# Kernel optimization log

Measured on AMD Instinct MI355X. Metric: run time of the kernel, lower is better.

## Reference

```python
import jax, jax.numpy as jnp
import numpy as np

N = 100000   # nodes
E = 1000000  # edges
DS = 16      # stage start/end scale-out vec dim
DC = 224     # raw context dim
CC = DS + DC + DS  # context_channels = 256
DM = 128     # stage_metrics_channels
H = (CC + DM) // 2  # 192 hidden of final_transform
OUT = 128    # out_channels (== DM, required by overwrite path)


def setup_inputs() -> dict:
    key = jax.random.key(0)
    ks = jax.random.split(key, 16)
    n = lambda k, shape, s=0.05: jax.random.normal(k, shape, jnp.float32) * s
    return {
        "edge_index": jax.random.randint(ks[0], (2, E), 0, N, dtype=jnp.int64),
        "stage_start": jax.random.normal(ks[1], (N, DS), jnp.float32),
        "stage_end": jax.random.normal(ks[2], (N, DS), jnp.float32),
        "context": jax.random.normal(ks[3], (N, DC), jnp.float32),
        "stage_metrics": jax.random.normal(ks[4], (N, DM), jnp.float32),
        "W_l": n(ks[5], (CC, CC)), "b_l": jnp.zeros((CC,), jnp.float32),
        "W_r": n(ks[6], (CC, CC)), "b_r": jnp.zeros((CC,), jnp.float32),
        "att": n(ks[7], (CC,)),
        "W1": n(ks[8], (CC + DM, H)), "b1": jnp.zeros((H,), jnp.float32),
        "W2": n(ks[9], (H, OUT)), "b2": jnp.zeros((OUT,), jnp.float32),
        "bias": jnp.zeros((OUT,), jnp.float32),
    }


def reference(edge_index, stage_start, stage_end, context, stage_metrics,
              W_l, b_l, W_r, b_r, att, W1, b1, W2, b2, bias):
    # node transform: [N, CC]
    nc = jnp.concatenate([stage_start, context, stage_end], axis=-1)
    cl = nc @ W_l + b_l  # source-side (j)
    cr = nc @ W_r + b_r  # target-side (i)

    src, dst = edge_index[0], edge_index[1]  # flow: source_to_target, aggregate by dst
    ci = cr[dst]                 # [E, CC] context_i
    cj = cl[src]                 # [E, CC] context_j
    mj = stage_metrics[src]      # [E, DM] metrics_j

    ctx = jax.nn.selu(ci + cj)
    ctx = jnp.where(jnp.all(mj == 0, axis=1, keepdims=True), 0.0, ctx)

    alpha = ctx @ att            # [E]
    mask = alpha != 0            # ~zero_indices

    # segment softmax over non-zero alphas, grouped by dst (PyG softmax: sub max, exp, /sum+eps)
    NEG = jnp.float32(-1e30)
    m = jax.ops.segment_max(jnp.where(mask, alpha, NEG), dst, num_segments=N)
    ex = jnp.where(mask, jnp.exp(alpha - m[dst]), 0.0)
    s = jax.ops.segment_sum(ex, dst, num_segments=N)
    a = jnp.where(mask, ex / (s[dst] + 1e-16), 0.0)

    # per-edge 2-layer SELU MLP
    h = jax.nn.selu(jnp.concatenate([ctx, mj], axis=-1) @ W1 + b1)  # [E, H]
    f = jax.nn.selu(h @ W2 + b2)                                    # [E, OUT]
    msg = jnp.where(mask[:, None], f * a[:, None], 0.0)

    # scatter-add aggregation to nodes
    out = jax.ops.segment_sum(msg, dst, num_segments=N)  # [N, OUT]

    # rows with all-zero aggregation are overwritten by stage_metrics; others get bias + sigmoid
    ovr = jnp.all(out == 0, axis=1, keepdims=True)
    return jnp.where(ovr, stage_metrics, jax.nn.sigmoid(out + bias))
```

## Files before the change

kernel.cpp:

```cpp
#include <hip/hip_runtime.h>
#include <hip/hip_bf16.h>
#include <math.h>

#define NN   100000
#define EE   1000000
#define CCH  256
#define DMC  128
#define HDC  192
#define OUTC 128
#define ET   32
#define MS   132
#define GS   391

typedef unsigned short u16;
using bf16x8 = __attribute__((ext_vector_type(8))) short;
using f32x4  = __attribute__((ext_vector_type(4))) float;
using u16x4  = __attribute__((ext_vector_type(4))) unsigned short;
using u16x8  = __attribute__((ext_vector_type(8))) unsigned short;

__device__ __forceinline__ float selu_f(float x) {
    const float sc = 1.0507009873554804934193349852946f;
    const float c1 = 1.7580993408473765792727863477367f;
    const float e = __expf(x);
    return x > 0.0f ? sc * x : __builtin_fmaf(c1, e, -c1);
}
__device__ __forceinline__ u16 f2bf(float f) {
    union { __hip_bfloat16 h; u16 u; } c;
    c.h = __float2bfloat16(f);
    return c.u;
}
__device__ __forceinline__ float bf2f(u16 h) {
    return __uint_as_float(((unsigned int)h) << 16);
}

__global__ __launch_bounds__(256, 2) void k_node_gemm(
    const float* __restrict__ ss, const float* __restrict__ se,
    const float* __restrict__ ctx, const u16* __restrict__ W0p,
    const float* __restrict__ bl, const float* __restrict__ br,
    u16* __restrict__ clb, u16* __restrict__ crb)
{
    __shared__ __align__(16) char Xs[64 * 512];
    const int tid = threadIdx.x;
    const int wave = tid >> 6, lane = tid & 63;
    const int node0 = blockIdx.x * 64;

    {
        const int r = lane;
        const int nd = min(node0 + r, NN - 1);
#pragma unroll
        for (int i = 0; i < 8; ++i) {
            const int c0 = wave * 64 + i * 8;
            float4 va, vb;
            {
                const int c = c0;
                if (c < 16)       va = *reinterpret_cast<const float4*>(ss + nd * 16 + c);
                else if (c < 240) va = *reinterpret_cast<const float4*>(ctx + (size_t)nd * 224 + (c - 16));
                else              va = *reinterpret_cast<const float4*>(se + nd * 16 + (c - 240));
            }
            {
                const int c = c0 + 4;
                if (c < 16)       vb = *reinterpret_cast<const float4*>(ss + nd * 16 + c);
                else if (c < 240) vb = *reinterpret_cast<const float4*>(ctx + (size_t)nd * 224 + (c - 16));
                else              vb = *reinterpret_cast<const float4*>(se + nd * 16 + (c - 240));
            }
            u16x8 v;
            v[0] = f2bf(va.x); v[1] = f2bf(va.y); v[2] = f2bf(va.z); v[3] = f2bf(va.w);
            v[4] = f2bf(vb.x); v[5] = f2bf(vb.y); v[6] = f2bf(vb.z); v[7] = f2bf(vb.w);
            *reinterpret_cast<u16x8*>(Xs + r * 512 + ((c0 * 2) ^ ((r & 7) << 4))) = v;
        }
    }
    __syncthreads();

    const int r16   = lane & 15;
    const int khalf = (lane >> 4) << 4;
    const int rbase = (lane >> 4) * 4;

    f32x4 acc[4][8];
#pragma unroll
    for (int m = 0; m < 4; ++m)
#pragma unroll
        for (int jj = 0; jj < 8; ++jj) acc[m][jj] = (f32x4){0.f, 0.f, 0.f, 0.f};

    for (int ks = 0; ks < 8; ++ks) {
        bf16x8 b[8];
#pragma unroll
        for (int jj = 0; jj < 8; ++jj)
            b[jj] = *reinterpret_cast<const bf16x8*>(
                W0p + (((size_t)(wave + 4 * jj) * 8 + ks) * 64 + lane) * 8);
        const int kb = ks * 64 + khalf;
#pragma unroll
        for (int m = 0; m < 4; ++m) {
            const int row = m * 16 + r16;
            const bf16x8 a = *reinterpret_cast<const bf16x8*>(
                Xs + row * 512 + (kb ^ ((row & 7) << 4)));
#pragma unroll
            for (int jj = 0; jj < 8; ++jj)
                acc[m][jj] = __builtin_amdgcn_mfma_f32_16x16x32_bf16(a, b[jj], acc[m][jj], 0, 0, 0);
        }
    }

#pragma unroll
    for (int jj = 0; jj < 8; ++jj) {
        const int nt = wave + 4 * jj;
        const bool isL = nt < 16;
        const int ncl = (isL ? nt * 16 : (nt - 16) * 16) + r16;
        const float bias = isL ? bl[ncl] : br[ncl];
        u16* base = (isL ? clb : crb) + ncl;
#pragma unroll
        for (int m = 0; m < 4; ++m)
#pragma unroll
            for (int rr = 0; rr < 4; ++rr) {
                const int node = node0 + m * 16 + rbase + rr;
                if (node < NN)
                    base[(size_t)node * CCH] = f2bf(acc[m][jj][rr] + bias);
            }
    }
}

__global__ __launch_bounds__(256) void k_convert(
    const float* __restrict__ in, u16* __restrict__ out, int n)
{
    const int i = (blockIdx.x * 256 + threadIdx.x) * 4;
    if (i < n) {
        const float4 v = *reinterpret_cast<const float4*>(in + i);
        u16x4 o; o[0] = f2bf(v.x); o[1] = f2bf(v.y); o[2] = f2bf(v.z); o[3] = f2bf(v.w);
        *reinterpret_cast<u16x4*>(out + i) = o;
    }
}

__global__ __launch_bounds__(64) void k_pack_w(
    const float* __restrict__ W, u16* __restrict__ out, int K, int N)
{
    const int f = blockIdx.x, lane = threadIdx.x;
    const int KS = K >> 5;
    const int nt = f / KS, ks = f - nt * KS;
    const int n = nt * 16 + (lane & 15);
    const int k0 = ks * 32 + (lane >> 4) * 8;
    u16x8 v;
#pragma unroll
    for (int j = 0; j < 8; ++j) v[j] = f2bf(W[(size_t)(k0 + j) * N + n]);
    *reinterpret_cast<u16x8*>(out + ((size_t)f * 64 + lane) * 8) = v;
}

__global__ __launch_bounds__(64) void k_pack_att(
    const float* __restrict__ att, u16* __restrict__ attp)
{
    const int ks = blockIdx.x;
    const int lane = threadIdx.x;
    const int nloc = lane & 15;
    const int k0 = ks * 32 + (lane >> 4) * 8;
    u16x8 v;
#pragma unroll
    for (int j = 0; j < 8; ++j) v[j] = f2bf((nloc == 0) ? att[k0 + j] : 0.f);
    *reinterpret_cast<u16x8*>(attp + ((size_t)ks * 64 + lane) * 8) = v;
}

__global__ __launch_bounds__(256) void k_hist(
    const int* __restrict__ ei, int* __restrict__ cnt)
{
    const int i = blockIdx.x * 256 + threadIdx.x;
    if (i < EE / 4) {
        const int4 d = *reinterpret_cast<const int4*>(ei + EE + i * 4);
        atomicAdd(&cnt[d.x], 1); atomicAdd(&cnt[d.y], 1);
        atomicAdd(&cnt[d.z], 1); atomicAdd(&cnt[d.w], 1);
    }
}

__global__ __launch_bounds__(256) void k_scan1(
    const int* __restrict__ cnt, int* __restrict__ bsum)
{
    const int i = blockIdx.x * 256 + threadIdx.x;
    int v = (i < NN) ? cnt[i] : 0;
#pragma unroll
    for (int o = 1; o < 64; o <<= 1) v += __shfl_xor(v, o);
    __shared__ int ws[4];
    if ((threadIdx.x & 63) == 0) ws[threadIdx.x >> 6] = v;
    __syncthreads();
    if (threadIdx.x == 0) bsum[blockIdx.x] = ws[0] + ws[1] + ws[2] + ws[3];
}

__global__ __launch_bounds__(512) void k_scan2(int* __restrict__ bsum)
{
    __shared__ int s[512];
    const int t = threadIdx.x;
    const int v = (t < GS) ? bsum[t] : 0;
    s[t] = v;
    __syncthreads();
    for (int o = 1; o < 512; o <<= 1) {
        const int u = (t >= o) ? s[t - o] : 0;
        __syncthreads();
        s[t] += u;
        __syncthreads();
    }
    if (t < GS) bsum[t] = s[t] - v;
}

__global__ __launch_bounds__(256) void k_scan3(
    const int* __restrict__ cnt, const int* __restrict__ bsum,
    int* __restrict__ cur)
{
    const int t = threadIdx.x;
    const int i = blockIdx.x * 256 + t;
    const int lane = t & 63, w = t >> 6;
    const int v = (i < NN) ? cnt[i] : 0;
    int x = v;
#pragma unroll
    for (int o = 1; o < 64; o <<= 1) {
        const int u = __shfl_up(x, o);
        if (lane >= o) x += u;
    }
    __shared__ int wsum[4];
    if (lane == 63) wsum[w] = x;
    __syncthreads();
    int off = bsum[blockIdx.x];
    for (int k2 = 0; k2 < w; ++k2) off += wsum[k2];
    if (i < NN) cur[i] = off + x - v;
}

__global__ __launch_bounds__(256) void k_scatter(
    const int* __restrict__ ei, int* __restrict__ cur,
    int* __restrict__ srcs, int* __restrict__ dsts)
{
    const int i = blockIdx.x * 256 + threadIdx.x;
    if (i < EE) {
        const int d = ei[EE + i];
        const int pos = atomicAdd(&cur[d], 1);
        srcs[pos] = ei[i];
        dsts[pos] = d;
    }
}

__global__ __launch_bounds__(256, 6) void k_edge_mlp(
    const int* __restrict__ srcs, const int* __restrict__ dsts,
    const u16* __restrict__ clb, const u16* __restrict__ crb,
    const u16* __restrict__ metb, const u16* __restrict__ attp,
    float* __restrict__ sb,
    const u16* __restrict__ W1p, const float* __restrict__ b1,
    const u16* __restrict__ W2p, const float* __restrict__ b2,
    float* __restrict__ dout)
{
    __shared__ __align__(16) char Xs[ET * 768];
    __shared__ int esrc[ET], edst[ET], flg[ET];
    __shared__ float exs[ET];

    const int tid  = threadIdx.x;
    const int wave = tid >> 6;
    const int lane = tid & 63;
    const int ebase = blockIdx.x * ET;

    if (tid < ET) {
        esrc[tid] = srcs[ebase + tid];
        edst[tid] = dsts[ebase + tid];
    }
    __syncthreads();

    u16x8 rv[4], lv[4], mv[2];
#pragma unroll
    for (int i = 0; i < 4; ++i) {
        const int k = tid + i * 256;
        const int t = k >> 5, c = k & 31;
        rv[i] = *reinterpret_cast<const u16x8*>(crb + (size_t)edst[t] * CCH + c * 8);
        lv[i] = *reinterpret_cast<const u16x8*>(clb + (size_t)esrc[t] * CCH + c * 8);
    }
#pragma unroll
    for (int i = 0; i < 2; ++i) {
        const int k = tid + i * 256;
        mv[i] = *reinterpret_cast<const u16x8*>(metb + (size_t)esrc[k >> 4] * DMC + (k & 15) * 8);
    }
#pragma unroll
    for (int i = 0; i < 4; ++i) {
        const int k = tid + i * 256;
        const int t = k >> 5, c = k & 31;
        u16x8 v;
#pragma unroll
        for (int j = 0; j < 8; ++j) v[j] = f2bf(selu_f(bf2f(rv[i][j]) + bf2f(lv[i][j])));
        *reinterpret_cast<u16x8*>(Xs + t * 768 + ((c * 16) ^ ((t & 7) << 4))) = v;
    }
#pragma unroll
    for (int i = 0; i < 2; ++i) {
        const int k = tid + i * 256;
        const int t = k >> 4, g = k & 15;
        unsigned ob = 0;
#pragma unroll
        for (int j = 0; j < 8; ++j) ob |= (unsigned)mv[i][j];
        const bool nz = (ob & 0x7fffu) != 0u;
        const unsigned long long bal = __ballot(nz);
        if ((lane & 15) == 0)
            flg[t] = (int)((bal >> ((lane >> 4) * 16)) & 0xFFFFull) != 0;
        *reinterpret_cast<u16x8*>(Xs + t * 768 + (((32 + g) * 16) ^ ((t & 7) << 4))) = mv[i];
    }
    __syncthreads();

    const int r16   = lane & 15;
    const int khalf = (lane >> 4) << 4;
    const int rbase = (lane >> 4) * 4;

    f32x4 acc[2][3];
    f32x4 acc3[2];
#pragma unroll
    for (int m = 0; m < 2; ++m) {
#pragma unroll
        for (int j = 0; j < 3; ++j) acc[m][j] = (f32x4){0.f, 0.f, 0.f, 0.f};
        acc3[m] = (f32x4){0.f, 0.f, 0.f, 0.f};
    }

    for (int ks = 0; ks < 12; ++ks) {
        bf16x8 b[3];
#pragma unroll
        for (int j = 0; j < 3; ++j)
            b[j] = *reinterpret_cast<const bf16x8*>(
                W1p + (((size_t)(wave + 4 * j) * 12 + ks) * 64 + lane) * 8);
        bf16x8 b3 = {};
        const bool doA = (wave == 0) && (ks < 8);
        if (doA)
            b3 = *reinterpret_cast<const bf16x8*>(attp + ((size_t)ks * 64 + lane) * 8);
        const int kb = ks * 64 + khalf;
#pragma unroll
        for (int m = 0; m < 2; ++m) {
            const int row = m * 16 + r16;
            const bf16x8 a = *reinterpret_cast<const bf16x8*>(
                Xs + row * 768 + (kb ^ ((row & 7) << 4)));
#pragma unroll
            for (int j = 0; j < 3; ++j)
                acc[m][j] = __builtin_amdgcn_mfma_f32_16x16x32_bf16(a, b[j], acc[m][j], 0, 0, 0);
            if (doA)
                acc3[m] = __builtin_amdgcn_mfma_f32_16x16x32_bf16(a, b3, acc3[m], 0, 0, 0);
        }
    }

    if (wave == 0 && r16 == 0) {
        const int hi = lane >> 4;
#pragma unroll
        for (int m = 0; m < 2; ++m)
#pragma unroll
            for (int r = 0; r < 4; ++r) {
                const int e = m * 16 + hi * 4 + r;
                const float al = acc3[m][r];
                exs[e] = (flg[e] && al != 0.f) ? __expf(al) : 0.f;
            }
    }
    __syncthreads();

#pragma unroll
    for (int j = 0; j < 3; ++j) {
        const int n = (wave + 4 * j) * 16 + r16;
        const float bb = b1[n];
#pragma unroll
        for (int m = 0; m < 2; ++m)
#pragma unroll
            for (int r = 0; r < 4; ++r) {
                const int row = m * 16 + rbase + r;
                *reinterpret_cast<u16*>(Xs + row * 384 + ((n * 2) ^ ((row & 7) << 4))) =
                    f2bf(selu_f(acc[m][j][r] + bb));
            }
    }
    __syncthreads();

    f32x4 acc2[2][2];
#pragma unroll
    for (int m = 0; m < 2; ++m)
#pragma unroll
        for (int j = 0; j < 2; ++j) acc2[m][j] = (f32x4){0.f, 0.f, 0.f, 0.f};

    for (int ks = 0; ks < 6; ++ks) {
        bf16x8 b[2];
#pragma unroll
        for (int j = 0; j < 2; ++j)
            b[j] = *reinterpret_cast<const bf16x8*>(
                W2p + (((size_t)(wave + 4 * j) * 6 + ks) * 64 + lane) * 8);
        const int kb = ks * 64 + khalf;
#pragma unroll
        for (int m = 0; m < 2; ++m) {
            const int row = m * 16 + r16;
            const bf16x8 a = *reinterpret_cast<const bf16x8*>(
                Xs + row * 384 + (kb ^ ((row & 7) << 4)));
#pragma unroll
            for (int j = 0; j < 2; ++j)
                acc2[m][j] = __builtin_amdgcn_mfma_f32_16x16x32_bf16(a, b[j], acc2[m][j], 0, 0, 0);
        }
    }
    __syncthreads();

    float* Ms = (float*)Xs;
#pragma unroll
    for (int j = 0; j < 2; ++j) {
        const int n = (wave + 4 * j) * 16 + r16;
        const float bb = b2[n];
#pragma unroll
        for (int m = 0; m < 2; ++m)
#pragma unroll
            for (int r = 0; r < 4; ++r) {
                const int e = m * 16 + rbase + r;
                Ms[e * MS + n] = selu_f(acc2[m][j][r] + bb) * exs[e];
            }
    }
    if (tid < ET) Ms[tid * MS + 128] = exs[tid];
    __syncthreads();

    {
        const int col = tid & 127;
        const int h = tid >> 7;
        const int r0 = h * 16;
        int cur_d = edst[r0];
        float s = Ms[r0 * MS + col];
        for (int r = r0 + 1; r < r0 + 16; ++r) {
            const int d = edst[r];
            const float v = Ms[r * MS + col];
            if (d != cur_d) {
                if (s != 0.f) atomicAdd(&dout[(size_t)cur_d * OUTC + col], s);
                cur_d = d; s = v;
            } else {
                s += v;
            }
        }
        if (s != 0.f) atomicAdd(&dout[(size_t)cur_d * OUTC + col], s);
    }
    if (tid < 2) {
        const int r0 = tid * 16;
        int cur_d = edst[r0];
        float s = Ms[r0 * MS + 128];
        for (int r = r0 + 1; r < r0 + 16; ++r) {
            const int d = edst[r];
            const float v = Ms[r * MS + 128];
            if (d != cur_d) {
                if (s != 0.f) atomicAdd(&sb[cur_d], s);
                cur_d = d; s = v;
            } else {
                s += v;
            }
        }
        if (s != 0.f) atomicAdd(&sb[cur_d], s);
    }
}

__global__ __launch_bounds__(256) void k_finalize(
    float* __restrict__ dout, const float* __restrict__ met,
    const float* __restrict__ bias, const float* __restrict__ sb)
{
    const int n = blockIdx.x * 4 + (threadIdx.x >> 6);
    const int lane = threadIdx.x & 63;
    const float a0 = dout[(size_t)n * OUTC + lane];
    const float a1 = dout[(size_t)n * OUTC + 64 + lane];
    const bool ovr = __all((a0 == 0.f) && (a1 == 0.f));
    float r0, r1;
    if (ovr) {
        r0 = met[(size_t)n * DMC + lane];
        r1 = met[(size_t)n * DMC + 64 + lane];
    } else {
        const float inv = 1.0f / (sb[n] + 1e-16f);
        r0 = 1.f / (1.f + __expf(-(a0 * inv + bias[lane])));
        r1 = 1.f / (1.f + __expf(-(a1 * inv + bias[64 + lane])));
    }
    dout[(size_t)n * OUTC + lane] = r0;
    dout[(size_t)n * OUTC + 64 + lane] = r1;
}

extern "C" void kernel_launch(void* const* d_in, const int* in_sizes, int n_in,
                              void* d_out, int out_size, void* d_ws, size_t ws_size,
                              hipStream_t stream)
{
    const int*   ei   = (const int*)d_in[0];
    const float* ss   = (const float*)d_in[1];
    const float* se   = (const float*)d_in[2];
    const float* ctx  = (const float*)d_in[3];
    const float* met  = (const float*)d_in[4];
    const float* Wl   = (const float*)d_in[5];
    const float* bl   = (const float*)d_in[6];
    const float* Wr   = (const float*)d_in[7];
    const float* br   = (const float*)d_in[8];
    const float* att  = (const float*)d_in[9];
    const float* W1   = (const float*)d_in[10];
    const float* b1   = (const float*)d_in[11];
    const float* W2   = (const float*)d_in[12];
    const float* b2   = (const float*)d_in[13];
    const float* bias = (const float*)d_in[14];

    u16* clb  = (u16*)d_ws;
    u16* crb  = clb  + (size_t)NN * CCH;
    u16* metb = crb  + (size_t)NN * CCH;
    u16* W1p  = metb + (size_t)NN * DMC;
    u16* W2p  = W1p  + (size_t)(CCH + DMC) * HDC;
    u16* W0p  = W2p  + (size_t)HDC * OUTC;
    float* sb = (float*)(W0p + (size_t)CCH * 512);
    int* cnt  = (int*)(sb + NN);
    int* cur  = cnt + NN;
    int* srcs = cur + NN;
    int* dsts = srcs + EE;
    int* bsum = dsts + EE;
    u16* attp = (u16*)(bsum + 512);

    float* dout = (float*)d_out;

    hipMemsetAsync(dout, 0, (size_t)NN * OUTC * sizeof(float), stream);
    hipMemsetAsync(sb, 0, (size_t)NN * sizeof(float), stream);
    hipMemsetAsync(cnt, 0, (size_t)NN * sizeof(int), stream);

    k_hist<<<(EE / 4 + 255) / 256, 256, 0, stream>>>(ei, cnt);
    k_scan1<<<GS, 256, 0, stream>>>(cnt, bsum);
    k_scan2<<<1, 512, 0, stream>>>(bsum);
    k_scan3<<<GS, 256, 0, stream>>>(cnt, bsum, cur);
    k_scatter<<<(EE + 255) / 256, 256, 0, stream>>>(ei, cur, srcs, dsts);

    k_pack_w<<<(CCH / 16) * (CCH / 32), 64, 0, stream>>>(Wl, W0p, CCH, CCH);
    k_pack_w<<<(CCH / 16) * (CCH / 32), 64, 0, stream>>>(Wr, W0p + (size_t)128 * 64 * 8, CCH, CCH);
    k_pack_w<<<(HDC / 16) * ((CCH + DMC) / 32), 64, 0, stream>>>(W1, W1p, CCH + DMC, HDC);
    k_pack_w<<<(OUTC / 16) * (HDC / 32), 64, 0, stream>>>(W2, W2p, HDC, OUTC);
    k_pack_att<<<8, 64, 0, stream>>>(att, attp);
    k_convert<<<(NN * DMC / 4 + 255) / 256, 256, 0, stream>>>(met, metb, NN * DMC);

    k_node_gemm<<<(NN + 63) / 64, 256, 0, stream>>>(ss, se, ctx, W0p, bl, br, clb, crb);
    k_edge_mlp<<<EE / ET, 256, 0, stream>>>(srcs, dsts, clb, crb, metb, attp, sb,
                                            W1p, b1, W2p, b2, dout);
    k_finalize<<<NN / 4, 256, 0, stream>>>(dout, met, bias, sb);
}
```

Baseline: 706.0 us.

## Double edge tile to 64 with 8-wave 2x4 layout and merge prep kernels

The edge MLP kernel now processes 64 edges per block with 512 threads arranged as a 2x4 wave grid. Each block's W1, W2 and att fragment loads are therefore shared across twice as many edges, cutting weight traffic per edge. Separately, the src/dst arrays are packed into int2, the four weight-pack launches and the att-pack launch are merged into one kernel, and two adjacent memsets are combined, all to save launches and loads. The larger tile doubles LDS use per block, which can lower how many blocks fit on a CU.

```diff
diff --git a/kernel.cpp b/kernel.cpp
--- a/kernel.cpp
+++ b/kernel.cpp
@@ -8,7 +8,7 @@
 #define DMC  128
 #define HDC  192
 #define OUTC 128
-#define ET   32
+#define ET   64
 #define MS   132
 #define GS   391
 
@@ -128,10 +128,10 @@
     }
 }
 
-__global__ __launch_bounds__(64) void k_pack_w(
-    const float* __restrict__ W, u16* __restrict__ out, int K, int N)
-{
-    const int f = blockIdx.x, lane = threadIdx.x;
+__device__ __forceinline__ void pack_frag(
+    const float* __restrict__ W, u16* __restrict__ out, int K, int N,
+    int f, int lane)
+{
     const int KS = K >> 5;
     const int nt = f / KS, ks = f - nt * KS;
     const int n = nt * 16 + (lane & 15);
@@ -142,17 +142,27 @@
     *reinterpret_cast<u16x8*>(out + ((size_t)f * 64 + lane) * 8) = v;
 }
 
-__global__ __launch_bounds__(64) void k_pack_att(
-    const float* __restrict__ att, u16* __restrict__ attp)
-{
-    const int ks = blockIdx.x;
-    const int lane = threadIdx.x;
-    const int nloc = lane & 15;
-    const int k0 = ks * 32 + (lane >> 4) * 8;
-    u16x8 v;
-#pragma unroll
-    for (int j = 0; j < 8; ++j) v[j] = f2bf((nloc == 0) ? att[k0 + j] : 0.f);
-    *reinterpret_cast<u16x8*>(attp + ((size_t)ks * 64 + lane) * 8) = v;
+__global__ __launch_bounds__(64) void k_pack_all(
+    const float* __restrict__ Wl, const float* __restrict__ Wr,
+    const float* __restrict__ W1, const float* __restrict__ W2,
+    const float* __restrict__ att,
+    u16* __restrict__ W0p, u16* __restrict__ W1p, u16* __restrict__ W2p,
+    u16* __restrict__ attp)
+{
+    const int b = blockIdx.x, lane = threadIdx.x;
+    if (b < 128)       pack_frag(Wl, W0p, CCH, CCH, b, lane);
+    else if (b < 256)  pack_frag(Wr, W0p + (size_t)128 * 64 * 8, CCH, CCH, b - 128, lane);
+    else if (b < 400)  pack_frag(W1, W1p, CCH + DMC, HDC, b - 256, lane);
+    else if (b < 448)  pack_frag(W2, W2p, HDC, OUTC, b - 400, lane);
+    else {
+        const int ks = b - 448;
+        const int nloc = lane & 15;
+        const int k0 = ks * 32 + (lane >> 4) * 8;
+        u16x8 v;
+#pragma unroll
+        for (int j = 0; j < 8; ++j) v[j] = f2bf((nloc == 0) ? att[k0 + j] : 0.f);
+        *reinterpret_cast<u16x8*>(attp + ((size_t)ks * 64 + lane) * 8) = v;
+    }
 }
 
 __global__ __launch_bounds__(256) void k_hist(
@@ -218,20 +228,18 @@
 }
 
 __global__ __launch_bounds__(256) void k_scatter(
-    const int* __restrict__ ei, int* __restrict__ cur,
-    int* __restrict__ srcs, int* __restrict__ dsts)
+    const int* __restrict__ ei, int* __restrict__ cur, int2* __restrict__ sd)
 {
     const int i = blockIdx.x * 256 + threadIdx.x;
     if (i < EE) {
         const int d = ei[EE + i];
         const int pos = atomicAdd(&cur[d], 1);
-        srcs[pos] = ei[i];
-        dsts[pos] = d;
-    }
-}
-
-__global__ __launch_bounds__(256, 6) void k_edge_mlp(
-    const int* __restrict__ srcs, const int* __restrict__ dsts,
+        sd[pos] = make_int2(ei[i], d);
+    }
+}
+
+__global__ __launch_bounds__(512, 6) void k_edge_mlp(
+    const int2* __restrict__ sd,
     const u16* __restrict__ clb, const u16* __restrict__ crb,
     const u16* __restrict__ metb, const u16* __restrict__ attp,
     float* __restrict__ sb,
@@ -246,30 +254,32 @@
     const int tid  = threadIdx.x;
     const int wave = tid >> 6;
     const int lane = tid & 63;
+    const int wm = wave >> 2, wn = wave & 3;
     const int ebase = blockIdx.x * ET;
 
     if (tid < ET) {
-        esrc[tid] = srcs[ebase + tid];
-        edst[tid] = dsts[ebase + tid];
+        const int2 p = sd[ebase + tid];
+        esrc[tid] = p.x;
+        edst[tid] = p.y;
     }
     __syncthreads();
 
     u16x8 rv[4], lv[4], mv[2];
 #pragma unroll
     for (int i = 0; i < 4; ++i) {
-        const int k = tid + i * 256;
+        const int k = tid + i * 512;
         const int t = k >> 5, c = k & 31;
         rv[i] = *reinterpret_cast<const u16x8*>(crb + (size_t)edst[t] * CCH + c * 8);
         lv[i] = *reinterpret_cast<const u16x8*>(clb + (size_t)esrc[t] * CCH + c * 8);
     }
 #pragma unroll
     for (int i = 0; i < 2; ++i) {
-        const int k = tid + i * 256;
+        const int k = tid + i * 512;
         mv[i] = *reinterpret_cast<const u16x8*>(metb + (size_t)esrc[k >> 4] * DMC + (k & 15) * 8);
     }
 #pragma unroll
     for (int i = 0; i < 4; ++i) {
-        const int k = tid + i * 256;
+        const int k = tid + i * 512;
         const int t = k >> 5, c = k & 31;
         u16x8 v;
 #pragma unroll
@@ -278,7 +288,7 @@
     }
 #pragma unroll
     for (int i = 0; i < 2; ++i) {
-        const int k = tid + i * 256;
+        const int k = tid + i * 512;
         const int t = k >> 4, g = k & 15;
         unsigned ob = 0;
 #pragma unroll
@@ -309,15 +319,15 @@
 #pragma unroll
         for (int j = 0; j < 3; ++j)
             b[j] = *reinterpret_cast<const bf16x8*>(
-                W1p + (((size_t)(wave + 4 * j) * 12 + ks) * 64 + lane) * 8);
+                W1p + (((size_t)(wn + 4 * j) * 12 + ks) * 64 + lane) * 8);
         bf16x8 b3 = {};
-        const bool doA = (wave == 0) && (ks < 8);
+        const bool doA = (wn == 0) && (ks < 8);
         if (doA)
             b3 = *reinterpret_cast<const bf16x8*>(attp + ((size_t)ks * 64 + lane) * 8);
         const int kb = ks * 64 + khalf;
 #pragma unroll
         for (int m = 0; m < 2; ++m) {
-            const int row = m * 16 + r16;
+            const int row = (wm * 2 + m) * 16 + r16;
             const bf16x8 a = *reinterpret_cast<const bf16x8*>(
                 Xs + row * 768 + (kb ^ ((row & 7) << 4)));
 #pragma unroll
@@ -328,13 +338,13 @@
         }
     }
 
-    if (wave == 0 && r16 == 0) {
+    if (wn == 0 && r16 == 0) {
         const int hi = lane >> 4;
 #pragma unroll
         for (int m = 0; m < 2; ++m)
 #pragma unroll
             for (int r = 0; r < 4; ++r) {
-                const int e = m * 16 + hi * 4 + r;
+                const int e = (wm * 2 + m) * 16 + hi * 4 + r;
                 const float al = acc3[m][r];
                 exs[e] = (flg[e] && al != 0.f) ? __expf(al) : 0.f;
             }
@@ -343,13 +353,13 @@
 
 #pragma unroll
     for (int j = 0; j < 3; ++j) {
-        const int n = (wave + 4 * j) * 16 + r16;
+        const int n = (wn + 4 * j) * 16 + r16;
         const float bb = b1[n];
 #pragma unroll
         for (int m = 0; m < 2; ++m)
 #pragma unroll
             for (int r = 0; r < 4; ++r) {
-                const int row = m * 16 + rbase + r;
+                const int row = (wm * 2 + m) * 16 + rbase + r;
                 *reinterpret_cast<u16*>(Xs + row * 384 + ((n * 2) ^ ((row & 7) << 4))) =
                     f2bf(selu_f(acc[m][j][r] + bb));
             }
@@ -367,11 +377,11 @@
 #pragma unroll
         for (int j = 0; j < 2; ++j)
             b[j] = *reinterpret_cast<const bf16x8*>(
-                W2p + (((size_t)(wave + 4 * j) * 6 + ks) * 64 + lane) * 8);
+                W2p + (((size_t)(wn + 4 * j) * 6 + ks) * 64 + lane) * 8);
         const int kb = ks * 64 + khalf;
 #pragma unroll
         for (int m = 0; m < 2; ++m) {
-            const int row = m * 16 + r16;
+            const int row = (wm * 2 + m) * 16 + r16;
             const bf16x8 a = *reinterpret_cast<const bf16x8*>(
                 Xs + row * 384 + (kb ^ ((row & 7) << 4)));
 #pragma unroll
@@ -384,13 +394,13 @@
     float* Ms = (float*)Xs;
 #pragma unroll
     for (int j = 0; j < 2; ++j) {
-        const int n = (wave + 4 * j) * 16 + r16;
+        const int n = (wn + 4 * j) * 16 + r16;
         const float bb = b2[n];
 #pragma unroll
         for (int m = 0; m < 2; ++m)
 #pragma unroll
             for (int r = 0; r < 4; ++r) {
-                const int e = m * 16 + rbase + r;
+                const int e = (wm * 2 + m) * 16 + rbase + r;
                 Ms[e * MS + n] = selu_f(acc2[m][j][r] + bb) * exs[e];
             }
     }
@@ -415,7 +425,7 @@
         }
         if (s != 0.f) atomicAdd(&dout[(size_t)cur_d * OUTC + col], s);
     }
-    if (tid < 2) {
+    if (tid < 4) {
         const int r0 = tid * 16;
         int cur_d = edst[r0];
         float s = Ms[r0 * MS + 128];
@@ -484,32 +494,26 @@
     float* sb = (float*)(W0p + (size_t)CCH * 512);
     int* cnt  = (int*)(sb + NN);
     int* cur  = cnt + NN;
-    int* srcs = cur + NN;
-    int* dsts = srcs + EE;
-    int* bsum = dsts + EE;
+    int2* sd  = (int2*)(cur + NN);
+    int* bsum = (int*)(sd + EE);
     u16* attp = (u16*)(bsum + 512);
 
     float* dout = (float*)d_out;
 
     hipMemsetAsync(dout, 0, (size_t)NN * OUTC * sizeof(float), stream);
-    hipMemsetAsync(sb, 0, (size_t)NN * sizeof(float), stream);
-    hipMemsetAsync(cnt, 0, (size_t)NN * sizeof(int), stream);
+    hipMemsetAsync(sb, 0, (size_t)NN * 2 * sizeof(float), stream);
 
     k_hist<<<(EE / 4 + 255) / 256, 256, 0, stream>>>(ei, cnt);
     k_scan1<<<GS, 256, 0, stream>>>(cnt, bsum);
     k_scan2<<<1, 512, 0, stream>>>(bsum);
     k_scan3<<<GS, 256, 0, stream>>>(cnt, bsum, cur);
-    k_scatter<<<(EE + 255) / 256, 256, 0, stream>>>(ei, cur, srcs, dsts);
-
-    k_pack_w<<<(CCH / 16) * (CCH / 32), 64, 0, stream>>>(Wl, W0p, CCH, CCH);
-    k_pack_w<<<(CCH / 16) * (CCH / 32), 64, 0, stream>>>(Wr, W0p + (size_t)128 * 64 * 8, CCH, CCH);
-    k_pack_w<<<(HDC / 16) * ((CCH + DMC) / 32), 64, 0, stream>>>(W1, W1p, CCH + DMC, HDC);
-    k_pack_w<<<(OUTC / 16) * (HDC / 32), 64, 0, stream>>>(W2, W2p, HDC, OUTC);
-    k_pack_att<<<8, 64, 0, stream>>>(att, attp);
+    k_scatter<<<(EE + 255) / 256, 256, 0, stream>>>(ei, cur, sd);
+
+    k_pack_all<<<456, 64, 0, stream>>>(Wl, Wr, W1, W2, att, W0p, W1p, W2p, attp);
     k_convert<<<(NN * DMC / 4 + 255) / 256, 256, 0, stream>>>(met, metb, NN * DMC);
 
     k_node_gemm<<<(NN + 63) / 64, 256, 0, stream>>>(ss, se, ctx, W0p, bl, br, clb, crb);
-    k_edge_mlp<<<EE / ET, 256, 0, stream>>>(srcs, dsts, clb, crb, metb, attp, sb,
+    k_edge_mlp<<<EE / ET, 512, 0, stream>>>(sd, clb, crb, metb, attp, sb,
                                             W1p, b1, W2p, b2, dout);
     k_finalize<<<NN / 4, 256, 0, stream>>>(dout, met, bias, sb);
 }
```

Measured after the change: 681.5 us. 3.5% less time.
